# Optimization experiments

Measured on AMD Instinct MI355X. Metric: run time of the kernel, lower is better.

Reference implementation:

```python
import math
import jax, jax.numpy as jnp
import numpy as np

B, S, T, C, CENC, H, D = 8, 4096, 77, 1280, 2048, 20, 64
STRENGTH = 0.5      # consistency_strength
ALPHA = 0.7         # self_keep_alpha
TOK_P = 0.15        # subject_token_top_p
POS_P = 0.3         # subject_patch_top_p
FIW = 0.5           # feature_injection_weight


def _topk_mask(scores, k):
    # scores: (B, L) -> bool mask (B, L) marking top-k per row
    Bx, L = scores.shape
    idx = jax.lax.top_k(scores, k)[1]
    return jnp.zeros((Bx, L), dtype=bool).at[jnp.arange(Bx)[:, None], idx].set(True)


def _mean_of_others(x):
    # y[i] = mean over j != i of x[j]
    Bx = x.shape[0]
    return (x.sum(axis=0, keepdims=True) - x) / (Bx - 1)


def setup_inputs() -> dict:
    key = jax.random.key(0)
    ks = jax.random.split(key, 7)
    return {
        "hidden_states": jax.random.normal(ks[0], (B, S, C), jnp.float32),
        "encoder_hidden_states": jax.random.normal(ks[1], (B, T, CENC), jnp.float32),
        "Wq": jax.random.normal(ks[2], (C, H * D), jnp.float32) * 0.02,
        "Wk": jax.random.normal(ks[3], (CENC, H * D), jnp.float32) * 0.02,
        "Wv": jax.random.normal(ks[4], (CENC, H * D), jnp.float32) * 0.02,
        "Wo": jax.random.normal(ks[5], (H * D, C), jnp.float32) * 0.02,
        "bo": jnp.zeros((C,), jnp.float32),
    }


def reference(hidden_states, encoder_hidden_states, Wq, Wk, Wv, Wo, bo):
    # project q/k/v and split heads: (B, H, L, D)
    q = (hidden_states @ Wq).reshape(B, S, H, D).transpose(0, 2, 1, 3)
    k = (encoder_hidden_states @ Wk).reshape(B, T, H, D).transpose(0, 2, 1, 3)
    v = (encoder_hidden_states @ Wv).reshape(B, T, H, D).transpose(0, 2, 1, 3)
    scale = 1.0 / math.sqrt(D)

    # first attention pass -> explicit probs (B, H, S, T)
    probs = jax.nn.softmax(jnp.einsum('bhsd,bhtd->bhst', q, k) * scale, axis=-1)

    # subject token mask: aggregate (B,H,S,T) -> (B,T), top-k
    tok_scores = probs.mean(axis=(1, 2))
    k_tok = max(1, int(math.ceil(T * TOK_P)))
    tok_mask = _topk_mask(tok_scores, k_tok)  # (B, T) bool

    # subject position mask: attention mass to subject tokens -> (B,S), top-k
    pos_scores = (probs * tok_mask[:, None, None, :].astype(probs.dtype)).sum(-1).mean(axis=1)
    k_pos = max(1, int(math.ceil(S * POS_P)))
    pos_mask = _topk_mask(pos_scores, k_pos)  # (B, S) bool

    # mask dropout: p = 0.0 -> no-op (deterministic)

    # cross-frame K/V mixing on subject tokens
    tm = tok_mask[:, None, :, None].astype(k.dtype)  # (B,1,T,1)
    def mix(x):
        mixed = ALPHA * x + (1.0 - ALPHA) * _mean_of_others(x)
        return x + STRENGTH * tm * (mixed - x)
    k2, v2 = mix(k), mix(v)

    # second attention pass with mixed K/V
    probs2 = jax.nn.softmax(jnp.einsum('bhsd,bhtd->bhst', q, k2) * scale, axis=-1)
    context = jnp.einsum('bhst,bhtd->bhsd', probs2, v2)

    # patch correspondence injection within subject region
    w = FIW * STRENGTH
    pm = pos_mask[:, None, :, None].astype(context.dtype)  # (B,1,S,1)
    context = context + w * pm * (_mean_of_others(context) - context)

    # merge heads, output projection, residual
    out = context.transpose(0, 2, 1, 3).reshape(B, S, H * D) @ Wo + bo + hidden_states
    return out
```

## Files before the change

kernel.cpp:

```cpp
#include <hip/hip_runtime.h>
#include <math.h>

#define B_    8
#define S_    4096
#define T_    77
#define C_    1280
#define CENC_ 2048
#define H_    20
#define D_    64
#define HD_   1280
#define M1_   (B_*S_)
#define MKV_  (B_*T_)
#define KTOK_ 12
#define KPOS_ 1229
#define SCALE_ 0.125f
#define CMIX_  0.15f
#define CINJ_  (0.25f/7.0f)

typedef __attribute__((ext_vector_type(8))) short bf16x8;
typedef __attribute__((ext_vector_type(4))) float f32x4;

#define AS_G __attribute__((address_space(1)))
#define AS_L __attribute__((address_space(3)))
#define MFMA16 __builtin_amdgcn_mfma_f32_16x16x32_bf16

__device__ inline unsigned short f2bf(float x)
{
    union { float f; unsigned u; } v; v.f = x;
    const unsigned r = v.u + 0x7FFFu + ((v.u >> 16) & 1u);
    return (unsigned short)(r >> 16);
}
__device__ inline float bf2f(unsigned short h)
{
    union { float f; unsigned u; } v; v.u = ((unsigned)h) << 16;
    return v.f;
}

__device__ inline void split_frag(const float* __restrict__ p, bf16x8& hi, bf16x8& lo)
{
    const float4 a = *(const float4*)p;
    const float4 b = *(const float4*)(p + 4);
    float f[8] = {a.x, a.y, a.z, a.w, b.x, b.y, b.z, b.w};
    #pragma unroll
    for (int e = 0; e < 8; ++e) {
        const unsigned short h = f2bf(f[e]);
        hi[e] = (short)h;
        lo[e] = (short)f2bf(f[e] - bf2f(h));
    }
}

__global__ __launch_bounds__(256)
void split_convert_kernel(const float* __restrict__ x, unsigned short* __restrict__ hi,
                          unsigned short* __restrict__ lo)
{
    const size_t i4 = (size_t)blockIdx.x * 256 + threadIdx.x;
    const float4 v = ((const float4*)x)[i4];
    ushort4 h, l;
    h.x = f2bf(v.x); l.x = f2bf(v.x - bf2f(h.x));
    h.y = f2bf(v.y); l.y = f2bf(v.y - bf2f(h.y));
    h.z = f2bf(v.z); l.z = f2bf(v.z - bf2f(h.z));
    h.w = f2bf(v.w); l.w = f2bf(v.w - bf2f(h.w));
    ((ushort4*)hi)[i4] = h;
    ((ushort4*)lo)[i4] = l;
}

__global__ __launch_bounds__(256)
void wsplitT_kernel(const float* __restrict__ W, unsigned short* __restrict__ Thi,
                    unsigned short* __restrict__ Tlo)
{
    __shared__ float tile[32][33];
    const int tx = threadIdx.x & 31, ty = threadIdx.x >> 5;
    const int n0 = blockIdx.x * 32, k0 = blockIdx.y * 32;
    #pragma unroll
    for (int i = 0; i < 4; ++i) {
        const int kk = ty + i * 8;
        tile[kk][tx] = W[(size_t)(k0 + kk) * 1280 + n0 + tx];
    }
    __syncthreads();
    #pragma unroll
    for (int i = 0; i < 4; ++i) {
        const int nn = ty + i * 8;
        const float v = tile[tx][nn];
        const unsigned short h = f2bf(v);
        const size_t oi = (size_t)(n0 + nn) * 1280 + k0 + tx;
        Thi[oi] = h;
        Tlo[oi] = f2bf(v - bf2f(h));
    }
}

__global__ __launch_bounds__(256)
void inject_convert_kernel(const float* __restrict__ ctx, const float* __restrict__ csum,
                           const float* __restrict__ posm, unsigned short* __restrict__ outb)
{
    const size_t i4 = (size_t)blockIdx.x * 256 + threadIdx.x;
    const int row = (int)(i4 / 320);
    const int c4  = (int)(i4 % 320);
    const float cf = posm[row] * CINJ_;
    const float am = 1.0f - 8.0f * cf;
    const float4 c  = ((const float4*)ctx)[i4];
    const float4 cs = ((const float4*)csum)[(size_t)(row & (S_ - 1)) * 320 + c4];
    ushort4 h;
    h.x = f2bf(c.x * am + cf * cs.x);
    h.y = f2bf(c.y * am + cf * cs.y);
    h.z = f2bf(c.z * am + cf * cs.z);
    h.w = f2bf(c.w * am + cf * cs.w);
    ((ushort4*)outb)[i4] = h;
}

__device__ inline void stage_tile(const unsigned short* __restrict__ gsrc,
                                  unsigned short* lds, int tid, int ldK,
                                  int row0, int k0)
{
    #pragma unroll
    for (int c0 = 0; c0 < 512; c0 += 256) {
        const int c = c0 + tid;
        const int rr = c >> 3;
        const int l  = (c & 7) ^ (rr & 7);
        const int row = 2 * rr + (l >> 2);
        const int j   = l & 3;
        const unsigned short* gp = gsrc + (size_t)(row0 + row) * ldK + k0 + j * 8;
        __builtin_amdgcn_global_load_lds((const AS_G void*)gp, (AS_L void*)(lds + (size_t)c * 8),
                                         16, 0, 0);
    }
}

__device__ inline int swz_off(int row, int quad)
{
    const int rr = row >> 1;
    const int pos = (((row & 1) << 2) | quad) ^ (rr & 7);
    return rr * 128 + pos * 16;
}

template<bool SPLIT, bool FUSE_OUT>
__global__ __launch_bounds__(256)
void mfma_gemm_kernel(const unsigned short* __restrict__ Ahi, const unsigned short* __restrict__ Alo,
                      const unsigned short* __restrict__ BhiT, const unsigned short* __restrict__ BloT,
                      float* __restrict__ Cout, int K,
                      const float* __restrict__ bias, const float* __restrict__ resid)
{
    __shared__ unsigned short sAhi[128 * 32];
    __shared__ unsigned short sBhi[128 * 32];
    __shared__ unsigned short sAlo[SPLIT ? 128 * 32 : 8];
    __shared__ unsigned short sBlo[SPLIT ? 128 * 32 : 8];

    const int tid  = threadIdx.x;
    const int lane = tid & 63;
    const int wave = tid >> 6;
    const int quad = lane >> 4;
    const int lrow = lane & 15;
    const int wm = (wave & 1) * 64;
    const int wn = (wave >> 1) * 64;

    const int bid = blockIdx.x;
    const int panel = bid / 320;
    const int r = bid % 320;
    const int n0 = (r >> 5) * 128;
    const int m0 = (panel * 32 + (r & 31)) * 128;

    f32x4 acc[4][4] = {};

    for (int k0 = 0; k0 < K; k0 += 32) {
        __syncthreads();
        stage_tile(Ahi,  sAhi, tid, K, m0, k0);
        stage_tile(BhiT, sBhi, tid, K, n0, k0);
        if constexpr (SPLIT) {
            stage_tile(Alo,  sAlo, tid, K, m0, k0);
            stage_tile(BloT, sBlo, tid, K, n0, k0);
        }
        __syncthreads();

        bf16x8 ah[4], bh[4];
        #pragma unroll
        for (int i = 0; i < 4; ++i) {
            const int ao = swz_off(wm + i * 16 + lrow, quad);
            const int bo = swz_off(wn + i * 16 + lrow, quad);
            ah[i] = *(const bf16x8*)((const char*)sAhi + ao);
            bh[i] = *(const bf16x8*)((const char*)sBhi + bo);
        }
        if constexpr (SPLIT) {
            bf16x8 al[4], bl[4];
            #pragma unroll
            for (int i = 0; i < 4; ++i) {
                const int ao = swz_off(wm + i * 16 + lrow, quad);
                const int bo = swz_off(wn + i * 16 + lrow, quad);
                al[i] = *(const bf16x8*)((const char*)sAlo + ao);
                bl[i] = *(const bf16x8*)((const char*)sBlo + bo);
            }
            #pragma unroll
            for (int mt = 0; mt < 4; ++mt)
                #pragma unroll
                for (int nt = 0; nt < 4; ++nt) {
                    acc[mt][nt] = MFMA16(ah[mt], bh[nt], acc[mt][nt], 0, 0, 0);
                    acc[mt][nt] = MFMA16(ah[mt], bl[nt], acc[mt][nt], 0, 0, 0);
                    acc[mt][nt] = MFMA16(al[mt], bh[nt], acc[mt][nt], 0, 0, 0);
                }
        } else {
            #pragma unroll
            for (int mt = 0; mt < 4; ++mt)
                #pragma unroll
                for (int nt = 0; nt < 4; ++nt)
                    acc[mt][nt] = MFMA16(ah[mt], bh[nt], acc[mt][nt], 0, 0, 0);
        }
    }

    #pragma unroll
    for (int mt = 0; mt < 4; ++mt) {
        #pragma unroll
        for (int nt = 0; nt < 4; ++nt) {
            const int col = n0 + wn + nt * 16 + lrow;
            #pragma unroll
            for (int r2 = 0; r2 < 4; ++r2) {
                const int row = m0 + wm + mt * 16 + quad * 4 + r2;
                float v = acc[mt][nt][r2];
                if constexpr (FUSE_OUT)
                    v += bias[col] + resid[(size_t)row * 1280 + col];
                Cout[(size_t)row * 1280 + col] = v;
            }
        }
    }
}

__global__ __launch_bounds__(256)
void gemm64_kernel(const float* __restrict__ A,
                   const float* __restrict__ B0, const float* __restrict__ B1,
                   float* __restrict__ C0, float* __restrict__ C1,
                   int M, int N, int K)
{
    const float* Bm = blockIdx.z ? B1 : B0;
    float* Cout = blockIdx.z ? C1 : C0;
    __shared__ float As[16][64];
    __shared__ float Bs[16][64];
    const int tid = threadIdx.x;
    const int n0 = blockIdx.x * 64;
    const int m0 = blockIdx.y * 64;
    const int tx = tid & 15, ty = tid >> 4;
    const int ar = tid >> 2;
    const int ak = (tid & 3) << 2;
    const int bk = tid >> 4;
    const int bn = (tid & 15) << 2;

    float acc[4][4] = {};
    const int arow = m0 + ar;
    const bool avalid = arow < M;
    const float* Ap = A + (size_t)arow * K + ak;
    const float* Bp = Bm + (size_t)bk * N + n0 + bn;

    for (int k0 = 0; k0 < K; k0 += 16) {
        const float4 a = avalid ? *(const float4*)(Ap + k0) : make_float4(0.f,0.f,0.f,0.f);
        const float4 b = *(const float4*)(Bp + (size_t)k0 * N);
        __syncthreads();
        As[ak+0][ar] = a.x; As[ak+1][ar] = a.y; As[ak+2][ar] = a.z; As[ak+3][ar] = a.w;
        *(float4*)&Bs[bk][bn] = b;
        __syncthreads();
        #pragma unroll
        for (int kk = 0; kk < 16; ++kk) {
            const float4 av = *(const float4*)&As[kk][ty*4];
            const float4 bv = *(const float4*)&Bs[kk][tx*4];
            const float arr[4] = {av.x, av.y, av.z, av.w};
            const float brr[4] = {bv.x, bv.y, bv.z, bv.w};
            #pragma unroll
            for (int r = 0; r < 4; ++r)
                #pragma unroll
                for (int c = 0; c < 4; ++c)
                    acc[r][c] = fmaf(arr[r], brr[c], acc[r][c]);
        }
    }
    #pragma unroll
    for (int r = 0; r < 4; ++r) {
        const int row = m0 + ty * 4 + r;
        if (row < M) {
            const float4 cv = make_float4(acc[r][0], acc[r][1], acc[r][2], acc[r][3]);
            *(float4*)(Cout + (size_t)row * N + n0 + tx * 4) = cv;
        }
    }
}

__device__ inline bool first_pair(float va, int ia, float vb, int ib)
{
    return (va > vb) || (va == vb && ia < ib);
}

__device__ inline void bitonic_desc(float* vals, int* idxs, int n, int tid, int nt)
{
    for (int k = 2; k <= n; k <<= 1) {
        for (int j = k >> 1; j > 0; j >>= 1) {
            __syncthreads();
            for (int i = tid; i < n; i += nt) {
                const int l = i ^ j;
                if (l > i) {
                    const float vi = vals[i], vl = vals[l];
                    const int   ii = idxs[i], il = idxs[l];
                    const bool up = (i & k) == 0;
                    const bool sw = up ? first_pair(vl, il, vi, ii)
                                       : first_pair(vi, ii, vl, il);
                    if (sw) { vals[i] = vl; vals[l] = vi; idxs[i] = il; idxs[l] = ii; }
                }
            }
        }
    }
    __syncthreads();
}

__global__ __launch_bounds__(256)
void pass_a_kernel(const float* __restrict__ q, const float* __restrict__ kbuf,
                   float* __restrict__ tokp)
{
    __shared__ unsigned short khi[80 * 64];
    __shared__ unsigned short klo[80 * 64];
    __shared__ float wsum[4][80];
    const int g = blockIdx.x;
    const int b = g / 320;
    const int rem = g % 320;
    const int h = rem >> 4;
    const int chunk = rem & 15;
    const int tid = threadIdx.x;

    for (int i = tid; i < 80 * 16; i += 256) {
        const int t = i >> 4, j = i & 15;
        float4 v = make_float4(0.f, 0.f, 0.f, 0.f);
        if (t < T_) v = *(const float4*)(kbuf + (size_t)(b * T_ + t) * HD_ + h * D_ + 4 * j);
        ushort4 hh, ll;
        hh.x = f2bf(v.x); ll.x = f2bf(v.x - bf2f(hh.x));
        hh.y = f2bf(v.y); ll.y = f2bf(v.y - bf2f(hh.y));
        hh.z = f2bf(v.z); ll.z = f2bf(v.z - bf2f(hh.z));
        hh.w = f2bf(v.w); ll.w = f2bf(v.w - bf2f(hh.w));
        const int byt = t * 128 + ((8 * j) ^ ((t & 7) << 4));
        *(ushort4*)((char*)khi + byt) = hh;
        *(ushort4*)((char*)klo + byt) = ll;
    }
    __syncthreads();

    const int wid = tid >> 6, lane = tid & 63;
    const int lrow = lane & 15, quad = lane >> 4;

    f32x4 tokacc[5] = {};
    for (int st = 0; st < 4; ++st) {
        const int s = chunk * 256 + wid * 64 + st * 16 + lrow;
        const float* qp = q + (size_t)(b * S_ + s) * HD_ + h * D_;
        bf16x8 qhi[2], qlo[2];
        #pragma unroll
        for (int ks = 0; ks < 2; ++ks)
            split_frag(qp + ks * 32 + quad * 8, qhi[ks], qlo[ks]);

        f32x4 acc[5] = {};
        #pragma unroll
        for (int nt = 0; nt < 5; ++nt) {
            #pragma unroll
            for (int ks = 0; ks < 2; ++ks) {
                const int krow = nt * 16 + lrow;
                const int byt = krow * 128 + ((64 * ks + 16 * quad) ^ ((krow & 7) << 4));
                const bf16x8 kh = *(const bf16x8*)((const char*)khi + byt);
                const bf16x8 kl = *(const bf16x8*)((const char*)klo + byt);
                acc[nt] = MFMA16(kh, qhi[ks], acc[nt], 0, 0, 0);
                acc[nt] = MFMA16(kh, qlo[ks], acc[nt], 0, 0, 0);
                acc[nt] = MFMA16(kl, qhi[ks], acc[nt], 0, 0, 0);
                acc[nt] = MFMA16(kl, qlo[ks], acc[nt], 0, 0, 0);
            }
        }
        float m = -1e30f;
        #pragma unroll
        for (int nt = 0; nt < 5; ++nt)
            #pragma unroll
            for (int r = 0; r < 4; ++r) {
                const int t = nt * 16 + quad * 4 + r;
                const float l = (t < T_) ? acc[nt][r] * SCALE_ : -1e30f;
                acc[nt][r] = l;
                m = fmaxf(m, l);
            }
        m = fmaxf(m, __shfl_xor(m, 16, 64));
        m = fmaxf(m, __shfl_xor(m, 32, 64));
        float Lp = 0.f;
        #pragma unroll
        for (int nt = 0; nt < 5; ++nt)
            #pragma unroll
            for (int r = 0; r < 4; ++r) {
                const float e = __expf(acc[nt][r] - m);
                acc[nt][r] = e;
                Lp += e;
            }
        float L = Lp + __shfl_xor(Lp, 16, 64);
        L += __shfl_xor(L, 32, 64);
        const float invL = 1.0f / L;
        #pragma unroll
        for (int nt = 0; nt < 5; ++nt)
            #pragma unroll
            for (int r = 0; r < 4; ++r)
                tokacc[nt][r] = fmaf(acc[nt][r], invL, tokacc[nt][r]);
    }
    #pragma unroll
    for (int nt = 0; nt < 5; ++nt)
        #pragma unroll
        for (int r = 0; r < 4; ++r) {
            float v = tokacc[nt][r];
            v += __shfl_xor(v, 1, 64);
            v += __shfl_xor(v, 2, 64);
            v += __shfl_xor(v, 4, 64);
            v += __shfl_xor(v, 8, 64);
            if (lrow == 0) wsum[wid][nt * 16 + quad * 4 + r] = v;
        }
    __syncthreads();
    for (int t = tid; t < T_; t += 256)
        tokp[(size_t)g * T_ + t] = (wsum[0][t] + wsum[1][t]) + (wsum[2][t] + wsum[3][t]);
}

__global__ __launch_bounds__(128)
void topk_tok_kernel(const float* __restrict__ tokp, float* __restrict__ tokm)
{
    __shared__ float vals[128];
    __shared__ int idxs[128];
    const int b = blockIdx.x, tid = threadIdx.x;
    float v = -1e30f;
    if (tid < T_) {
        float sm = 0.f;
        for (int j = 0; j < 320; ++j) sm += tokp[(size_t)(b * 320 + j) * T_ + tid];
        v = sm;
    }
    vals[tid] = v; idxs[tid] = tid;
    bitonic_desc(vals, idxs, 128, tid, 128);
    if (tid < T_) tokm[b * T_ + tid] = 0.f;
    __syncthreads();
    if (tid < KTOK_) tokm[b * T_ + idxs[tid]] = 1.0f;
}

__global__ __launch_bounds__(256)
void mix_kernel(const float* __restrict__ kbuf, const float* __restrict__ vbuf,
                const float* __restrict__ tokm,
                float* __restrict__ kd, float* __restrict__ v2)
{
    const int i = blockIdx.x * 256 + threadIdx.x;
    const int t = i / HD_;
    float ks = 0.f, vs = 0.f;
    #pragma unroll
    for (int b = 0; b < B_; ++b) {
        ks += kbuf[(size_t)b * T_ * HD_ + i];
        vs += vbuf[(size_t)b * T_ * HD_ + i];
    }
    #pragma unroll
    for (int b = 0; b < B_; ++b) {
        const size_t gi = (size_t)b * T_ * HD_ + i;
        const float msk = tokm[b * T_ + t];
        const float kx = kbuf[gi], vx = vbuf[gi];
        kd[gi] = CMIX_ * msk * ((ks - 8.f * kx) * (1.0f / 7.0f));
        v2[gi] = vx + CMIX_ * msk * ((vs - 8.f * vx) * (1.0f / 7.0f));
    }
}

__global__ __launch_bounds__(256)
void pass_bc_kernel(const float* __restrict__ q, const float* __restrict__ kbuf,
                    const float* __restrict__ kd, const float* __restrict__ v2,
                    const float* __restrict__ tokm,
                    float* __restrict__ posp, float* __restrict__ ctx)
{
    __shared__ unsigned short khi[80 * 64];
    __shared__ unsigned short klo[80 * 64];
    __shared__ unsigned short kdh[80 * 64];
    __shared__ unsigned short vThi[64 * 88];
    __shared__ unsigned short vTlo[64 * 88];
    __shared__ unsigned short vguard[128];
    __shared__ unsigned short Pbuf[4][2][16 * 40];
    __shared__ float smaskf[80];

    const int g = blockIdx.x;
    const int b = g / 320;
    const int rem = g % 320;
    const int h = rem >> 4;
    const int chunk = rem & 15;
    const int tid = threadIdx.x;

    for (int i = tid; i < 80 * 16; i += 256) {
        const int t = i >> 4, j = i & 15;
        float4 vk = make_float4(0.f, 0.f, 0.f, 0.f);
        float4 vd = make_float4(0.f, 0.f, 0.f, 0.f);
        if (t < T_) {
            const size_t gi = (size_t)(b * T_ + t) * HD_ + h * D_ + 4 * j;
            vk = *(const float4*)(kbuf + gi);
            vd = *(const float4*)(kd + gi);
        }
        ushort4 hh, ll, dd;
        hh.x = f2bf(vk.x); ll.x = f2bf(vk.x - bf2f(hh.x)); dd.x = f2bf(vd.x);
        hh.y = f2bf(vk.y); ll.y = f2bf(vk.y - bf2f(hh.y)); dd.y = f2bf(vd.y);
        hh.z = f2bf(vk.z); ll.z = f2bf(vk.z - bf2f(hh.z)); dd.z = f2bf(vd.z);
        hh.w = f2bf(vk.w); ll.w = f2bf(vk.w - bf2f(hh.w)); dd.w = f2bf(vd.w);
        const int byt = t * 128 + ((8 * j) ^ ((t & 7) << 4));
        *(ushort4*)((char*)khi + byt) = hh;
        *(ushort4*)((char*)klo + byt) = ll;
        *(ushort4*)((char*)kdh + byt) = dd;
    }
    for (int i = tid; i < 64 * 22; i += 256) {
        const int d = i / 22, jg = i - d * 22;
        float vv[4];
        #pragma unroll
        for (int r = 0; r < 4; ++r) {
            const int t = 4 * jg + r;
            vv[r] = (t < T_) ? v2[(size_t)(b * T_ + t) * HD_ + h * D_ + d] : 0.f;
        }
        ushort4 hh, ll;
        hh.x = f2bf(vv[0]); ll.x = f2bf(vv[0] - bf2f(hh.x));
        hh.y = f2bf(vv[1]); ll.y = f2bf(vv[1] - bf2f(hh.y));
        hh.z = f2bf(vv[2]); ll.z = f2bf(vv[2] - bf2f(hh.z));
        hh.w = f2bf(vv[3]); ll.w = f2bf(vv[3] - bf2f(hh.w));
        const int byt = d * 176 + 8 * jg;
        *(ushort4*)((char*)vThi + byt) = hh;
        *(ushort4*)((char*)vTlo + byt) = ll;
    }
    for (int t = tid; t < 80; t += 256) smaskf[t] = (t < T_) ? tokm[b * T_ + t] : 0.f;
    for (int i = tid; i < 128; i += 256) vguard[i] = 0;
    __syncthreads();

    const int wid = tid >> 6, lane = tid & 63;
    const int lrow = lane & 15, quad = lane >> 4;
    unsigned short* Ph = &Pbuf[wid][0][0];
    unsigned short* Pl = &Pbuf[wid][1][0];

    float smv[5][4];
    #pragma unroll
    for (int nt = 0; nt < 5; ++nt)
        #pragma unroll
        for (int r = 0; r < 4; ++r)
            smv[nt][r] = smaskf[nt * 16 + quad * 4 + r];

    for (int st = 0; st < 4; ++st) {
        const int s = chunk * 256 + wid * 64 + st * 16 + lrow;
        const float* qp = q + (size_t)(b * S_ + s) * HD_ + h * D_;
        bf16x8 qhi[2], qlo[2];
        #pragma unroll
        for (int ks = 0; ks < 2; ++ks)
            split_frag(qp + ks * 32 + quad * 8, qhi[ks], qlo[ks]);

        f32x4 acc1[5] = {}, accd[5] = {};
        #pragma unroll
        for (int nt = 0; nt < 5; ++nt) {
            #pragma unroll
            for (int ks = 0; ks < 2; ++ks) {
                const int krow = nt * 16 + lrow;
                const int byt = krow * 128 + ((64 * ks + 16 * quad) ^ ((krow & 7) << 4));
                const bf16x8 kh = *(const bf16x8*)((const char*)khi + byt);
                const bf16x8 kl = *(const bf16x8*)((const char*)klo + byt);
                const bf16x8 kdv = *(const bf16x8*)((const char*)kdh + byt);
                acc1[nt] = MFMA16(kh, qhi[ks], acc1[nt], 0, 0, 0);
                acc1[nt] = MFMA16(kh, qlo[ks], acc1[nt], 0, 0, 0);
                acc1[nt] = MFMA16(kl, qhi[ks], acc1[nt], 0, 0, 0);
                acc1[nt] = MFMA16(kl, qlo[ks], acc1[nt], 0, 0, 0);
                accd[nt] = MFMA16(kdv, qhi[ks], accd[nt], 0, 0, 0);
            }
        }

        float m1 = -1e30f, m2 = -1e30f;
        f32x4 l2v[5];
        #pragma unroll
        for (int nt = 0; nt < 5; ++nt)
            #pragma unroll
            for (int r = 0; r < 4; ++r) {
                const int t = nt * 16 + quad * 4 + r;
                const bool valid = t < T_;
                const float l1 = valid ? acc1[nt][r] * SCALE_ : -1e30f;
                const float l2 = valid ? l1 + accd[nt][r] * SCALE_ : -1e30f;
                acc1[nt][r] = l1;
                l2v[nt][r] = l2;
                m1 = fmaxf(m1, l1);
                m2 = fmaxf(m2, l2);
            }
        m1 = fmaxf(m1, __shfl_xor(m1, 16, 64));
        m1 = fmaxf(m1, __shfl_xor(m1, 32, 64));
        m2 = fmaxf(m2, __shfl_xor(m2, 16, 64));
        m2 = fmaxf(m2, __shfl_xor(m2, 32, 64));
        float L1p = 0.f, Smp = 0.f, L2p = 0.f;
        #pragma unroll
        for (int nt = 0; nt < 5; ++nt)
            #pragma unroll
            for (int r = 0; r < 4; ++r) {
                const float e1 = __expf(acc1[nt][r] - m1);
                L1p += e1;
                Smp = fmaf(e1, smv[nt][r], Smp);
                const float e2 = __expf(l2v[nt][r] - m2);
                l2v[nt][r] = e2;
                L2p += e2;
            }
        float L1 = L1p + __shfl_xor(L1p, 16, 64); L1 += __shfl_xor(L1, 32, 64);
        float Sm = Smp + __shfl_xor(Smp, 16, 64); Sm += __shfl_xor(Sm, 32, 64);
        float L2 = L2p + __shfl_xor(L2p, 16, 64); L2 += __shfl_xor(L2, 32, 64);
        if (quad == 0) posp[(size_t)(b * H_ + h) * S_ + s] = Sm / L1;
        const float invL2 = 1.0f / L2;
        #pragma unroll
        for (int nt = 0; nt < 5; ++nt)
            #pragma unroll
            for (int r = 0; r < 4; ++r)
                l2v[nt][r] *= invL2;

        f32x4 pv[4] = {};
        #pragma unroll
        for (int ks = 0; ks < 3; ++ks) {
            asm volatile("s_waitcnt lgkmcnt(0)" ::: "memory");
            __builtin_amdgcn_sched_barrier(0);
            #pragma unroll
            for (int half = 0; half < 2; ++half) {
                const int nt = 2 * ks + half;
                ushort4 ph = {0, 0, 0, 0}, plw = {0, 0, 0, 0};
                if (nt < 5) {
                    ph.x = f2bf(l2v[nt][0]); plw.x = f2bf(l2v[nt][0] - bf2f(ph.x));
                    ph.y = f2bf(l2v[nt][1]); plw.y = f2bf(l2v[nt][1] - bf2f(ph.y));
                    ph.z = f2bf(l2v[nt][2]); plw.z = f2bf(l2v[nt][2] - bf2f(ph.z));
                    ph.w = f2bf(l2v[nt][3]); plw.w = f2bf(l2v[nt][3] - bf2f(ph.w));
                }
                const int pb = lrow * 80 + 32 * half + 8 * quad;
                *(ushort4*)((char*)Ph + pb) = ph;
                *(ushort4*)((char*)Pl + pb) = plw;
            }
            asm volatile("s_waitcnt lgkmcnt(0)" ::: "memory");
            __builtin_amdgcn_sched_barrier(0);
            const bf16x8 pH = *(const bf16x8*)((const char*)Ph + lrow * 80 + quad * 16);
            const bf16x8 pL = *(const bf16x8*)((const char*)Pl + lrow * 80 + quad * 16);
            #pragma unroll
            for (int mt = 0; mt < 4; ++mt) {
                const int vb = (mt * 16 + lrow) * 176 + 64 * ks + 16 * quad;
                const bf16x8 vH = *(const bf16x8*)((const char*)vThi + vb);
                const bf16x8 vL = *(const bf16x8*)((const char*)vTlo + vb);
                pv[mt] = MFMA16(vH, pH, pv[mt], 0, 0, 0);
                pv[mt] = MFMA16(vH, pL, pv[mt], 0, 0, 0);
                pv[mt] = MFMA16(vL, pH, pv[mt], 0, 0, 0);
            }
        }
        float* cp = ctx + (size_t)(b * S_ + s) * HD_ + h * D_;
        #pragma unroll
        for (int mt = 0; mt < 4; ++mt) {
            const float4 o = make_float4(pv[mt][0], pv[mt][1], pv[mt][2], pv[mt][3]);
            *(float4*)(cp + mt * 16 + quad * 4) = o;
        }
    }
}

__global__ __launch_bounds__(1024)
void topk_pos_kernel(const float* __restrict__ posp, float* __restrict__ posm)
{
    __shared__ float vals[S_];
    __shared__ int idxs[S_];
    const int b = blockIdx.x, tid = threadIdx.x;
    for (int s = tid; s < S_; s += 1024) {
        float sm = 0.f;
        for (int h = 0; h < H_; ++h) sm += posp[(size_t)(b * H_ + h) * S_ + s];
        vals[s] = sm; idxs[s] = s;
    }
    bitonic_desc(vals, idxs, S_, tid, 1024);
    for (int s = tid; s < S_; s += 1024) posm[b * S_ + s] = 0.f;
    __syncthreads();
    for (int i = tid; i < KPOS_; i += 1024) posm[b * S_ + idxs[i]] = 1.0f;
}

__global__ __launch_bounds__(256)
void ctxsum_kernel(const float* __restrict__ ctx, float* __restrict__ csum)
{
    const size_t i = (size_t)blockIdx.x * 256 + threadIdx.x;
    const float4* c = (const float4*)ctx;
    float4 a = c[i];
    #pragma unroll
    for (int b = 1; b < B_; ++b) {
        const float4 x = c[(size_t)b * (S_ * HD_ / 4) + i];
        a.x += x.x; a.y += x.y; a.z += x.z; a.w += x.w;
    }
    ((float4*)csum)[i] = a;
}

extern "C" void kernel_launch(void* const* d_in, const int* in_sizes, int n_in,
                              void* d_out, int out_size, void* d_ws, size_t ws_size,
                              hipStream_t stream)
{
    const float* hidden = (const float*)d_in[0];
    const float* enc    = (const float*)d_in[1];
    const float* Wq     = (const float*)d_in[2];
    const float* Wk     = (const float*)d_in[3];
    const float* Wv     = (const float*)d_in[4];
    const float* Wo     = (const float*)d_in[5];
    const float* bo     = (const float*)d_in[6];
    float* out = (float*)d_out;

    char* w = (char*)d_ws;
    float* q    = (float*)w; w += (size_t)M1_ * HD_ * 4;
    float* ctx  = (float*)w; w += (size_t)M1_ * HD_ * 4;
    float* kbuf = (float*)w; w += (size_t)B_ * T_ * HD_ * 4;
    float* vbuf = (float*)w; w += (size_t)B_ * T_ * HD_ * 4;
    float* kd   = (float*)w; w += (size_t)B_ * T_ * HD_ * 4;
    float* v2   = (float*)w; w += (size_t)B_ * T_ * HD_ * 4;
    float* csum = (float*)w; w += (size_t)S_ * HD_ * 4;
    float* tokp = (float*)w; w += (size_t)2560 * T_ * 4;
    float* posp = (float*)w; w += (size_t)B_ * H_ * S_ * 4;
    float* tokm = (float*)w; w += (size_t)B_ * T_ * 4;
    float* posm = (float*)w; w += (size_t)B_ * S_ * 4;
    unsigned short* Ahi   = (unsigned short*)w; w += (size_t)M1_ * HD_ * 2;
    unsigned short* Alo   = (unsigned short*)w; w += (size_t)M1_ * HD_ * 2;
    unsigned short* ctxb  = (unsigned short*)w; w += (size_t)M1_ * HD_ * 2;
    unsigned short* WqhiT = (unsigned short*)w; w += (size_t)C_ * HD_ * 2;
    unsigned short* WqloT = (unsigned short*)w; w += (size_t)C_ * HD_ * 2;
    unsigned short* WohiT = (unsigned short*)w; w += (size_t)HD_ * C_ * 2;
    unsigned short* WoloT = (unsigned short*)w; w += (size_t)HD_ * C_ * 2;
    (void)ws_size; (void)in_sizes; (void)n_in; (void)out_size;

    split_convert_kernel<<<M1_ * HD_ / 4 / 256, 256, 0, stream>>>(hidden, Ahi, Alo);
    wsplitT_kernel<<<dim3(40, 40), 256, 0, stream>>>(Wq, WqhiT, WqloT);
    wsplitT_kernel<<<dim3(40, 40), 256, 0, stream>>>(Wo, WohiT, WoloT);
    mfma_gemm_kernel<true, false><<<2560, 256, 0, stream>>>(
        Ahi, Alo, WqhiT, WqloT, q, C_, nullptr, nullptr);
    gemm64_kernel<<<dim3(20, 10, 2), 256, 0, stream>>>(
        enc, Wk, Wv, kbuf, vbuf, MKV_, HD_, CENC_);
    pass_a_kernel<<<2560, 256, 0, stream>>>(q, kbuf, tokp);
    topk_tok_kernel<<<8, 128, 0, stream>>>(tokp, tokm);
    mix_kernel<<<385, 256, 0, stream>>>(kbuf, vbuf, tokm, kd, v2);
    pass_bc_kernel<<<2560, 256, 0, stream>>>(q, kbuf, kd, v2, tokm, posp, ctx);
    topk_pos_kernel<<<8, 1024, 0, stream>>>(posp, posm);
    ctxsum_kernel<<<S_ * HD_ / 4 / 256, 256, 0, stream>>>(ctx, csum);
    inject_convert_kernel<<<M1_ * HD_ / 4 / 256, 256, 0, stream>>>(ctx, csum, posm, ctxb);
    mfma_gemm_kernel<false, true><<<2560, 256, 0, stream>>>(
        ctxb, nullptr, WohiT, nullptr, out, HD_, bo, hidden);
}
```

Before: 1.545 ms.

## Double-buffer LDS tiles in MFMA GEMM with async global-to-LDS prefetch

Double-buffers the shared-memory A/B tiles so the loads for the next K step are issued before the MFMAs on the current tile. Manual vmcnt waits and raw s_barrier replace the two __syncthreads per iteration, which is meant to hide global load latency behind matrix math. It also raises wave priority around the MFMA block. The cost is doubled LDS per block, which may reduce occupancy, and the vmcnt counts depend on how many loads stage_tile issues, so a wrong count would be fragile.

```diff
diff --git a/kernel.cpp b/kernel.cpp
--- a/kernel.cpp
+++ b/kernel.cpp
@@ -23,6 +23,7 @@
 #define AS_G __attribute__((address_space(1)))
 #define AS_L __attribute__((address_space(3)))
 #define MFMA16 __builtin_amdgcn_mfma_f32_16x16x32_bf16
+#define SBAR() asm volatile("s_barrier" ::: "memory")
 
 __device__ inline unsigned short f2bf(float x)
 {
@@ -138,10 +139,10 @@
                       float* __restrict__ Cout, int K,
                       const float* __restrict__ bias, const float* __restrict__ resid)
 {
-    __shared__ unsigned short sAhi[128 * 32];
-    __shared__ unsigned short sBhi[128 * 32];
-    __shared__ unsigned short sAlo[SPLIT ? 128 * 32 : 8];
-    __shared__ unsigned short sBlo[SPLIT ? 128 * 32 : 8];
+    __shared__ unsigned short sAhi[2][128 * 32];
+    __shared__ unsigned short sBhi[2][128 * 32];
+    __shared__ unsigned short sAlo[SPLIT ? 2 : 1][SPLIT ? 128 * 32 : 8];
+    __shared__ unsigned short sBlo[SPLIT ? 2 : 1][SPLIT ? 128 * 32 : 8];
 
     const int tid  = threadIdx.x;
     const int lane = tid & 63;
@@ -159,23 +160,38 @@
 
     f32x4 acc[4][4] = {};
 
-    for (int k0 = 0; k0 < K; k0 += 32) {
-        __syncthreads();
-        stage_tile(Ahi,  sAhi, tid, K, m0, k0);
-        stage_tile(BhiT, sBhi, tid, K, n0, k0);
+    auto stage_all = [&](int bufi, int k0) {
+        stage_tile(Ahi,  sAhi[bufi], tid, K, m0, k0);
+        stage_tile(BhiT, sBhi[bufi], tid, K, n0, k0);
         if constexpr (SPLIT) {
-            stage_tile(Alo,  sAlo, tid, K, m0, k0);
-            stage_tile(BloT, sBlo, tid, K, n0, k0);
-        }
-        __syncthreads();
+            stage_tile(Alo,  sAlo[bufi], tid, K, m0, k0);
+            stage_tile(BloT, sBlo[bufi], tid, K, n0, k0);
+        }
+    };
+
+    const int NK = K >> 5;
+    stage_all(0, 0);
+
+    for (int kt = 0; kt < NK; ++kt) {
+        const int cur = kt & 1;
+        if (kt + 1 < NK) {
+            stage_all(cur ^ 1, (kt + 1) << 5);
+            if constexpr (SPLIT)
+                asm volatile("s_waitcnt vmcnt(8)" ::: "memory");
+            else
+                asm volatile("s_waitcnt vmcnt(4)" ::: "memory");
+        } else {
+            asm volatile("s_waitcnt vmcnt(0)" ::: "memory");
+        }
+        SBAR();
 
         bf16x8 ah[4], bh[4];
         #pragma unroll
         for (int i = 0; i < 4; ++i) {
             const int ao = swz_off(wm + i * 16 + lrow, quad);
             const int bo = swz_off(wn + i * 16 + lrow, quad);
-            ah[i] = *(const bf16x8*)((const char*)sAhi + ao);
-            bh[i] = *(const bf16x8*)((const char*)sBhi + bo);
+            ah[i] = *(const bf16x8*)((const char*)sAhi[cur] + ao);
+            bh[i] = *(const bf16x8*)((const char*)sBhi[cur] + bo);
         }
         if constexpr (SPLIT) {
             bf16x8 al[4], bl[4];
@@ -183,9 +199,10 @@
             for (int i = 0; i < 4; ++i) {
                 const int ao = swz_off(wm + i * 16 + lrow, quad);
                 const int bo = swz_off(wn + i * 16 + lrow, quad);
-                al[i] = *(const bf16x8*)((const char*)sAlo + ao);
-                bl[i] = *(const bf16x8*)((const char*)sBlo + bo);
-            }
+                al[i] = *(const bf16x8*)((const char*)sAlo[cur] + ao);
+                bl[i] = *(const bf16x8*)((const char*)sBlo[cur] + bo);
+            }
+            __builtin_amdgcn_s_setprio(1);
             #pragma unroll
             for (int mt = 0; mt < 4; ++mt)
                 #pragma unroll
@@ -194,13 +211,17 @@
                     acc[mt][nt] = MFMA16(ah[mt], bl[nt], acc[mt][nt], 0, 0, 0);
                     acc[mt][nt] = MFMA16(al[mt], bh[nt], acc[mt][nt], 0, 0, 0);
                 }
+            __builtin_amdgcn_s_setprio(0);
         } else {
+            __builtin_amdgcn_s_setprio(1);
             #pragma unroll
             for (int mt = 0; mt < 4; ++mt)
                 #pragma unroll
                 for (int nt = 0; nt < 4; ++nt)
                     acc[mt][nt] = MFMA16(ah[mt], bh[nt], acc[mt][nt], 0, 0, 0);
-        }
+            __builtin_amdgcn_s_setprio(0);
+        }
+        SBAR();
     }
 
     #pragma unroll
```

After: 1.535 ms. Within noise of the previous version (-0.7%).
